# Optimization experiments

Hardware: AMD Instinct MI355X
Metric: run time of the kernel (lower is better)

Reference implementation:

```python
import jax, jax.numpy as jnp
import numpy as np

N = 100000
E = 1600000
IN_DIM = 256
HID = 64


def setup_inputs() -> dict:
    key = jax.random.key(0)
    k1, k2, k3 = jax.random.split(key, 3)
    x = jax.random.normal(k1, (N, IN_DIM), dtype=jnp.float32)
    edge_index = jax.random.randint(k2, (2, E), 0, N, dtype=jnp.int64)
    # glorot-ish init for GCNConv weight, zero bias (PyG default)
    W = jax.random.normal(k3, (IN_DIM, HID), dtype=jnp.float32) * (1.0 / np.sqrt(IN_DIM))
    b = jnp.zeros((HID,), dtype=jnp.float32)
    return {"x": x, "edge_index": edge_index, "W": W, "b": b}


def reference(x, edge_index, W, b):
    # GCNConv: out = D^{-1/2} (A + I) D^{-1/2} (X W) + b
    n = x.shape[0]
    # add self-loops
    loop = jnp.arange(n, dtype=edge_index.dtype)
    src = jnp.concatenate([edge_index[0], loop])  # [E+N]
    dst = jnp.concatenate([edge_index[1], loop])  # [E+N]
    # degree of target nodes (incl. self-loops)
    deg = jax.ops.segment_sum(jnp.ones_like(dst, dtype=x.dtype), dst, num_segments=n)
    dinv = jnp.where(deg > 0, jax.lax.rsqrt(deg), 0.0)  # deg^{-1/2}, inf->0
    norm = dinv[src] * dinv[dst]  # [E+N]
    h = x @ W  # [N, HID] transform before aggregation
    msg = h[src] * norm[:, None]  # gather + scale, [E+N, HID]
    out = jax.ops.segment_sum(msg, dst, num_segments=n)  # scatter-add
    return out + b
```

## Files before the change

kernel.cpp:

```cpp
#include <hip/hip_runtime.h>

typedef float floatx4 __attribute__((ext_vector_type(4)));
typedef short s16x8 __attribute__((ext_vector_type(8)));

#define WG 256
#define NBUCK 512
#define BSH 8
#define EBLK 512
#define CAP 8192

__device__ inline unsigned pack_bf16_rne(float a, float b) {
    unsigned ua = __float_as_uint(a), ub = __float_as_uint(b);
    ua = (ua + 0x7FFFu + ((ua >> 16) & 1u)) >> 16;
    ub = (ub + 0x7FFFu + ((ub >> 16) & 1u)) >> 16;
    return ua | (ub << 16);
}

union FragU {
    unsigned u[4];
    uint4 q;
    s16x8 v;
};

__global__ __launch_bounds__(WG) void k_build(const void* __restrict__ ei, int* __restrict__ cursor,
                                              unsigned* __restrict__ ebuf, int E) {
    __shared__ int h[NBUCK];
    __shared__ int base[NBUCK];
    __shared__ int s32flag;
    const int t = threadIdx.x;
    if (t == 0) s32flag = 0;
    for (int i = t; i < NBUCK; i += WG) h[i] = 0;
    __syncthreads();
    {
        const int* w = (const int*)ei;
        int nz = 0;
        for (int j = t; j < 4096; j += WG) nz |= (w[2 * j + 1] != 0);
        if (nz) atomicOr(&s32flag, 1);
    }
    __syncthreads();
    const bool i32 = (s32flag != 0);
    const int chunk = (E + EBLK - 1) / EBLK;
    const int s = blockIdx.x * chunk;
    const int eend = min(E, s + chunk);
    if (i32) {
        const int* pd = (const int*)ei + E;
        for (int e = s + t; e < eend; e += WG) atomicAdd(&h[pd[e] >> BSH], 1);
    } else {
        const long long* pd = (const long long*)ei + E;
        for (int e = s + t; e < eend; e += WG) atomicAdd(&h[(int)pd[e] >> BSH], 1);
    }
    __syncthreads();
    for (int i = t; i < NBUCK; i += WG) {
        int c = h[i];
        base[i] = c ? atomicAdd(&cursor[i], c) : 0;
        h[i] = 0;
    }
    __syncthreads();
    for (int e = s + t; e < eend; e += WG) {
        int sN, dN;
        if (i32) {
            const int* p = (const int*)ei;
            sN = p[e];
            dN = p[E + e];
        } else {
            const long long* p = (const long long*)ei;
            sN = (int)p[e];
            dN = (int)p[(long long)E + e];
        }
        int bkt = dN >> BSH;
        int pos = base[bkt] + atomicAdd(&h[bkt], 1);
        if (pos < CAP) ebuf[(size_t)bkt * CAP + pos] = (unsigned)sN | ((unsigned)(dN & 255) << 24);
    }
}

__global__ __launch_bounds__(WG) void k_mid(const unsigned* __restrict__ ebuf, const int* __restrict__ cursor,
                                            int* __restrict__ off, int* __restrict__ srcs,
                                            float* __restrict__ dinv,
                                            const float* __restrict__ x, const float* __restrict__ W,
                                            unsigned short* __restrict__ g, int N, int nbuse) {
    __shared__ unsigned smem[2048 * 4];
    const int t = threadIdx.x;

    if ((int)blockIdx.x < nbuse) {
        int* red = (int*)smem;
        int* h = red + 256;
        int* sc = h + 256;
        int* cur = sc + 256;
        const int b = blockIdx.x;
        const int node0 = b << BSH;
        const int rows = min(256, N - node0);
        int part = 0;
        for (int i = t; i < b; i += WG) part += min(cursor[i], CAP);
        red[t] = part;
        h[t] = 0;
        __syncthreads();
        for (int d = WG / 2; d > 0; d >>= 1) {
            if (t < d) red[t] += red[t + d];
            __syncthreads();
        }
        const int ebase = red[0];
        const int cnt = min(cursor[b], CAP);
        const unsigned* eb = ebuf + (size_t)b * CAP;
        for (int j = t; j < cnt; j += WG) atomicAdd(&h[eb[j] >> 24], 1);
        __syncthreads();
        const int deg = (t < rows) ? h[t] + 1 : 0;
        sc[t] = deg;
        __syncthreads();
        for (int d = 1; d < 256; d <<= 1) {
            int a = (t >= d) ? sc[t - d] : 0;
            __syncthreads();
            sc[t] += a;
            __syncthreads();
        }
        const int basef = ebase + node0;
        const int local = sc[t] - deg;
        if (t < rows) {
            off[node0 + t] = basef + local;
            srcs[basef + local] = node0 + t;
            cur[t] = local + 1;
            dinv[node0 + t] = rsqrtf((float)deg);
        }
        if (b == nbuse - 1 && t == 0) off[N] = ebase + cnt + N;
        __syncthreads();
        for (int j = t; j < cnt; j += WG) {
            unsigned w = eb[j];
            int dl = (int)(w >> 24);
            int pos = basef + atomicAdd(&cur[dl], 1);
            srcs[pos] = (int)(w & 0xFFFFFFu);
        }
    } else {
        const int bb = blockIdx.x - nbuse;
        for (int q = t; q < 2048; q += WG) {
            const int kb = q >> 8, nt = (q >> 6) & 3, ln = q & 63;
            const int quad = ln >> 4, l15 = ln & 15;
            const int col = nt * 16 + l15;
            const int krow = kb * 32 + quad * 8;
            unsigned up[4];
#pragma unroll
            for (int p = 0; p < 4; p++) {
                float a = W[(krow + 2 * p) * 64 + col];
                float b2 = W[(krow + 2 * p + 1) * 64 + col];
                up[p] = pack_bf16_rne(a, b2);
            }
            uint4 pk = {up[0], up[1], up[2], up[3]};
            *(uint4*)(&smem[q * 4]) = pk;
        }
        __syncthreads();

        const int wv = t >> 6;
        const int lane = t & 63;
        const int quad = lane >> 4, l15 = lane & 15;

        long long arow = (long long)bb * 64 + wv * 16 + l15;
        if (arow >= N) arow = N - 1;
        const float* xr = x + arow * 256 + quad * 8;

        floatx4 xv[8][2];
#pragma unroll
        for (int kb = 0; kb < 8; kb++) {
            xv[kb][0] = *(const floatx4*)(xr + kb * 32);
            xv[kb][1] = *(const floatx4*)(xr + kb * 32 + 4);
        }

        floatx4 acc[4];
#pragma unroll
        for (int nt = 0; nt < 4; nt++) acc[nt] = 0.f;

#pragma unroll
        for (int kb = 0; kb < 8; kb++) {
            FragU a;
            a.u[0] = pack_bf16_rne(xv[kb][0][0], xv[kb][0][1]);
            a.u[1] = pack_bf16_rne(xv[kb][0][2], xv[kb][0][3]);
            a.u[2] = pack_bf16_rne(xv[kb][1][0], xv[kb][1][1]);
            a.u[3] = pack_bf16_rne(xv[kb][1][2], xv[kb][1][3]);
#pragma unroll
            for (int nt = 0; nt < 4; nt++) {
                FragU b2;
                b2.q = *(const uint4*)(&smem[((kb * 4 + nt) * 64 + lane) * 4]);
                acc[nt] = __builtin_amdgcn_mfma_f32_16x16x32_bf16(a.v, b2.v, acc[nt], 0, 0, 0);
            }
        }

        const long long orow0 = (long long)bb * 64 + wv * 16 + quad * 4;
#pragma unroll
        for (int r = 0; r < 4; r++) {
            const long long orow = orow0 + r;
            if (orow < N) {
#pragma unroll
                for (int nt = 0; nt < 4; nt++) {
                    float v = acc[nt][r];
                    unsigned uv = __float_as_uint(v);
                    uv = (uv + 0x7FFFu + ((uv >> 16) & 1u)) >> 16;
                    g[orow * 64 + nt * 16 + l15] = (unsigned short)uv;
                }
            }
        }
    }
}

__global__ __launch_bounds__(WG) void k_gather(const unsigned short* __restrict__ g,
                                               const int* __restrict__ off, const int* __restrict__ srcs,
                                               const float* __restrict__ dinv, const float* __restrict__ bias,
                                               float* __restrict__ out, int N) {
    int wid = (blockIdx.x * WG + threadIdx.x) >> 6;
    int lane = threadIdx.x & 63;
    if (wid >= N) return;
    int grp = lane >> 3;
    int c8 = (lane & 7) * 8;
    int e0 = off[wid], e1 = off[wid + 1];
    float a0 = 0.f, a1 = 0.f, a2 = 0.f, a3 = 0.f, a4 = 0.f, a5 = 0.f, a6 = 0.f, a7 = 0.f;
    int e = e0 + grp;
    int s = (e < e1) ? srcs[e] : 0;
    while (e < e1) {
        int en = e + 8;
        int sn = (en < e1) ? srcs[en] : 0;
        float ds = dinv[s];
        uint4 v = *(const uint4*)(g + (long long)s * 64 + c8);
        a0 += ds * __uint_as_float(v.x << 16);
        a1 += ds * __uint_as_float(v.x & 0xFFFF0000u);
        a2 += ds * __uint_as_float(v.y << 16);
        a3 += ds * __uint_as_float(v.y & 0xFFFF0000u);
        a4 += ds * __uint_as_float(v.z << 16);
        a5 += ds * __uint_as_float(v.z & 0xFFFF0000u);
        a6 += ds * __uint_as_float(v.w << 16);
        a7 += ds * __uint_as_float(v.w & 0xFFFF0000u);
        s = sn;
        e = en;
    }
#pragma unroll
    for (int m = 8; m <= 32; m <<= 1) {
        a0 += __shfl_xor(a0, m, 64);
        a1 += __shfl_xor(a1, m, 64);
        a2 += __shfl_xor(a2, m, 64);
        a3 += __shfl_xor(a3, m, 64);
        a4 += __shfl_xor(a4, m, 64);
        a5 += __shfl_xor(a5, m, 64);
        a6 += __shfl_xor(a6, m, 64);
        a7 += __shfl_xor(a7, m, 64);
    }
    if (grp == 0) {
        float d = dinv[wid];
        const floatx4 b0 = *(const floatx4*)(bias + c8);
        const floatx4 b1 = *(const floatx4*)(bias + c8 + 4);
        floatx4 o0, o1;
        o0[0] = d * a0 + b0[0];
        o0[1] = d * a1 + b0[1];
        o0[2] = d * a2 + b0[2];
        o0[3] = d * a3 + b0[3];
        o1[0] = d * a4 + b1[0];
        o1[1] = d * a5 + b1[1];
        o1[2] = d * a6 + b1[2];
        o1[3] = d * a7 + b1[3];
        *(floatx4*)(out + (long long)wid * 64 + c8) = o0;
        *(floatx4*)(out + (long long)wid * 64 + c8 + 4) = o1;
    }
}

extern "C" void kernel_launch(void* const* d_in, const int* in_sizes, int n_in,
                              void* d_out, int out_size, void* d_ws, size_t ws_size,
                              hipStream_t stream) {
    const float* x = (const float*)d_in[0];
    const void* ei = d_in[1];
    const float* W = (const float*)d_in[2];
    const float* b = (const float*)d_in[3];
    float* out = (float*)d_out;

    const int N = in_sizes[0] / 256;
    const int E = in_sizes[1] / 2;
    const int NBUSE = (N + 255) >> BSH;
    const int GEMMB = (N + 63) / 64;

    char* ws = (char*)d_ws;
    size_t o = 0;
    auto alloc = [&](size_t bytes) -> void* {
        void* p = ws + o;
        o += (bytes + 255) & ~(size_t)255;
        return p;
    };
    float* dinv = (float*)alloc((size_t)N * 4);
    unsigned short* g = (unsigned short*)alloc((size_t)N * 64 * 2);
    unsigned* ebuf = (unsigned*)alloc((size_t)NBUSE * CAP * 4);
    int* cursor = (int*)alloc((size_t)NBUCK * 4);
    int* off = (int*)alloc((size_t)(N + 1) * 4);
    int* srcs = (int*)alloc((size_t)(E + N) * 4);
    if (o > ws_size) return;

    hipMemsetAsync(cursor, 0, (size_t)NBUCK * 4, stream);
    k_build<<<EBLK, WG, 0, stream>>>(ei, cursor, ebuf, E);
    k_mid<<<NBUSE + GEMMB, WG, 0, stream>>>(ebuf, cursor, off, srcs, dinv, x, W, g, N, NBUSE);
    k_gather<<<(N * 64 + WG - 1) / WG, WG, 0, stream>>>(g, off, srcs, dinv, b, out, N);
}
```

Before: 270.1 us.

## Overlap edge bucketing with GEMM and prepack W in a separate kernel

Reorganizes the launch schedule so the edge bucketing pass runs in the same kernel as the X·W MFMA GEMM blocks, and the CSR construction moves into its own kernel afterward. W is converted to a bf16 MFMA fragment layout once by a small prepack kernel, which also zeroes the cursor array in place of the memset. GEMM blocks then copy the packed W into LDS after issuing their x loads. The aim is to overlap the atomic-heavy bucketing with the bandwidth-heavy GEMM and to stop every GEMM block from repacking W. The cost is one extra kernel launch, and the two kinds of blocks now share one grid.

```diff
diff --git a/kernel.cpp b/kernel.cpp
--- a/kernel.cpp
+++ b/kernel.cpp
@@ -22,131 +22,82 @@
     s16x8 v;
 };
 
-__global__ __launch_bounds__(WG) void k_build(const void* __restrict__ ei, int* __restrict__ cursor,
-                                              unsigned* __restrict__ ebuf, int E) {
-    __shared__ int h[NBUCK];
-    __shared__ int base[NBUCK];
-    __shared__ int s32flag;
-    const int t = threadIdx.x;
-    if (t == 0) s32flag = 0;
-    for (int i = t; i < NBUCK; i += WG) h[i] = 0;
-    __syncthreads();
-    {
-        const int* w = (const int*)ei;
-        int nz = 0;
-        for (int j = t; j < 4096; j += WG) nz |= (w[2 * j + 1] != 0);
-        if (nz) atomicOr(&s32flag, 1);
-    }
-    __syncthreads();
-    const bool i32 = (s32flag != 0);
-    const int chunk = (E + EBLK - 1) / EBLK;
-    const int s = blockIdx.x * chunk;
-    const int eend = min(E, s + chunk);
-    if (i32) {
-        const int* pd = (const int*)ei + E;
-        for (int e = s + t; e < eend; e += WG) atomicAdd(&h[pd[e] >> BSH], 1);
-    } else {
-        const long long* pd = (const long long*)ei + E;
-        for (int e = s + t; e < eend; e += WG) atomicAdd(&h[(int)pd[e] >> BSH], 1);
-    }
-    __syncthreads();
-    for (int i = t; i < NBUCK; i += WG) {
-        int c = h[i];
-        base[i] = c ? atomicAdd(&cursor[i], c) : 0;
-        h[i] = 0;
-    }
-    __syncthreads();
-    for (int e = s + t; e < eend; e += WG) {
-        int sN, dN;
-        if (i32) {
-            const int* p = (const int*)ei;
-            sN = p[e];
-            dN = p[E + e];
-        } else {
-            const long long* p = (const long long*)ei;
-            sN = (int)p[e];
-            dN = (int)p[(long long)E + e];
-        }
-        int bkt = dN >> BSH;
-        int pos = base[bkt] + atomicAdd(&h[bkt], 1);
-        if (pos < CAP) ebuf[(size_t)bkt * CAP + pos] = (unsigned)sN | ((unsigned)(dN & 255) << 24);
-    }
-}
-
-__global__ __launch_bounds__(WG) void k_mid(const unsigned* __restrict__ ebuf, const int* __restrict__ cursor,
-                                            int* __restrict__ off, int* __restrict__ srcs,
-                                            float* __restrict__ dinv,
-                                            const float* __restrict__ x, const float* __restrict__ W,
-                                            unsigned short* __restrict__ g, int N, int nbuse) {
+__global__ __launch_bounds__(WG) void k_packw(const float* __restrict__ W,
+                                              uint4* __restrict__ wpack,
+                                              int* __restrict__ cursor) {
+    const int q = blockIdx.x * WG + threadIdx.x;
+    if (q < NBUCK) cursor[q] = 0;
+    const int kb = q >> 8, nt = (q >> 6) & 3, ln = q & 63;
+    const int quad = ln >> 4, l15 = ln & 15;
+    const int col = nt * 16 + l15;
+    const int krow = kb * 32 + quad * 8;
+    unsigned up[4];
+#pragma unroll
+    for (int p = 0; p < 4; p++) {
+        float a = W[(krow + 2 * p) * 64 + col];
+        float b2 = W[(krow + 2 * p + 1) * 64 + col];
+        up[p] = pack_bf16_rne(a, b2);
+    }
+    uint4 pk = {up[0], up[1], up[2], up[3]};
+    wpack[q] = pk;
+}
+
+__global__ __launch_bounds__(WG) void k_main(const void* __restrict__ ei, int* __restrict__ cursor,
+                                             unsigned* __restrict__ ebuf, int E,
+                                             const float* __restrict__ x, const uint4* __restrict__ wpack,
+                                             unsigned short* __restrict__ g, int N) {
     __shared__ unsigned smem[2048 * 4];
     const int t = threadIdx.x;
 
-    if ((int)blockIdx.x < nbuse) {
-        int* red = (int*)smem;
-        int* h = red + 256;
-        int* sc = h + 256;
-        int* cur = sc + 256;
-        const int b = blockIdx.x;
-        const int node0 = b << BSH;
-        const int rows = min(256, N - node0);
-        int part = 0;
-        for (int i = t; i < b; i += WG) part += min(cursor[i], CAP);
-        red[t] = part;
-        h[t] = 0;
-        __syncthreads();
-        for (int d = WG / 2; d > 0; d >>= 1) {
-            if (t < d) red[t] += red[t + d];
-            __syncthreads();
-        }
-        const int ebase = red[0];
-        const int cnt = min(cursor[b], CAP);
-        const unsigned* eb = ebuf + (size_t)b * CAP;
-        for (int j = t; j < cnt; j += WG) atomicAdd(&h[eb[j] >> 24], 1);
-        __syncthreads();
-        const int deg = (t < rows) ? h[t] + 1 : 0;
-        sc[t] = deg;
-        __syncthreads();
-        for (int d = 1; d < 256; d <<= 1) {
-            int a = (t >= d) ? sc[t - d] : 0;
-            __syncthreads();
-            sc[t] += a;
-            __syncthreads();
-        }
-        const int basef = ebase + node0;
-        const int local = sc[t] - deg;
-        if (t < rows) {
-            off[node0 + t] = basef + local;
-            srcs[basef + local] = node0 + t;
-            cur[t] = local + 1;
-            dinv[node0 + t] = rsqrtf((float)deg);
-        }
-        if (b == nbuse - 1 && t == 0) off[N] = ebase + cnt + N;
-        __syncthreads();
-        for (int j = t; j < cnt; j += WG) {
-            unsigned w = eb[j];
-            int dl = (int)(w >> 24);
-            int pos = basef + atomicAdd(&cur[dl], 1);
-            srcs[pos] = (int)(w & 0xFFFFFFu);
+    if ((int)blockIdx.x < EBLK) {
+        int* h = (int*)smem;
+        int* base = h + NBUCK;
+        int* s32flag = base + NBUCK;
+        if (t == 0) *s32flag = 0;
+        for (int i = t; i < NBUCK; i += WG) h[i] = 0;
+        __syncthreads();
+        {
+            const int* w = (const int*)ei;
+            int nz = 0;
+            for (int j = t; j < 4096; j += WG) nz |= (w[2 * j + 1] != 0);
+            if (nz) atomicOr(s32flag, 1);
+        }
+        __syncthreads();
+        const bool i32 = (*s32flag != 0);
+        const int chunk = (E + EBLK - 1) / EBLK;
+        const int s = blockIdx.x * chunk;
+        const int eend = min(E, s + chunk);
+        if (i32) {
+            const int* pd = (const int*)ei + E;
+            for (int e = s + t; e < eend; e += WG) atomicAdd(&h[pd[e] >> BSH], 1);
+        } else {
+            const long long* pd = (const long long*)ei + E;
+            for (int e = s + t; e < eend; e += WG) atomicAdd(&h[(int)pd[e] >> BSH], 1);
+        }
+        __syncthreads();
+        for (int i = t; i < NBUCK; i += WG) {
+            int c = h[i];
+            base[i] = c ? atomicAdd(&cursor[i], c) : 0;
+            h[i] = 0;
+        }
+        __syncthreads();
+        for (int e = s + t; e < eend; e += WG) {
+            int sN, dN;
+            if (i32) {
+                const int* p = (const int*)ei;
+                sN = p[e];
+                dN = p[E + e];
+            } else {
+                const long long* p = (const long long*)ei;
+                sN = (int)p[e];
+                dN = (int)p[(long long)E + e];
+            }
+            int bkt = dN >> BSH;
+            int pos = base[bkt] + atomicAdd(&h[bkt], 1);
+            if (pos < CAP) ebuf[(size_t)bkt * CAP + pos] = (unsigned)sN | ((unsigned)(dN & 255) << 24);
         }
     } else {
-        const int bb = blockIdx.x - nbuse;
-        for (int q = t; q < 2048; q += WG) {
-            const int kb = q >> 8, nt = (q >> 6) & 3, ln = q & 63;
-            const int quad = ln >> 4, l15 = ln & 15;
-            const int col = nt * 16 + l15;
-            const int krow = kb * 32 + quad * 8;
-            unsigned up[4];
-#pragma unroll
-            for (int p = 0; p < 4; p++) {
-                float a = W[(krow + 2 * p) * 64 + col];
-                float b2 = W[(krow + 2 * p + 1) * 64 + col];
-                up[p] = pack_bf16_rne(a, b2);
-            }
-            uint4 pk = {up[0], up[1], up[2], up[3]};
-            *(uint4*)(&smem[q * 4]) = pk;
-        }
-        __syncthreads();
-
+        const int bb = blockIdx.x - EBLK;
         const int wv = t >> 6;
         const int lane = t & 63;
         const int quad = lane >> 4, l15 = lane & 15;
@@ -161,6 +112,14 @@
             xv[kb][0] = *(const floatx4*)(xr + kb * 32);
             xv[kb][1] = *(const floatx4*)(xr + kb * 32 + 4);
         }
+        __builtin_amdgcn_sched_barrier(0);
+
+#pragma unroll
+        for (int i = 0; i < 8; i++) {
+            const int q = i * WG + t;
+            ((uint4*)smem)[q] = wpack[q];
+        }
+        __syncthreads();
 
         floatx4 acc[4];
 #pragma unroll
@@ -195,6 +154,58 @@
                 }
             }
         }
+    }
+}
+
+__global__ __launch_bounds__(WG) void k_csr(const unsigned* __restrict__ ebuf, const int* __restrict__ cursor,
+                                            int* __restrict__ off, int* __restrict__ srcs,
+                                            float* __restrict__ dinv, int N, int nbuse) {
+    __shared__ int red[256];
+    __shared__ int h[256];
+    __shared__ int sc[256];
+    __shared__ int cur[256];
+    const int t = threadIdx.x;
+    const int b = blockIdx.x;
+    const int node0 = b << BSH;
+    const int rows = min(256, N - node0);
+    int part = 0;
+    for (int i = t; i < b; i += WG) part += min(cursor[i], CAP);
+    red[t] = part;
+    h[t] = 0;
+    __syncthreads();
+    for (int d = WG / 2; d > 0; d >>= 1) {
+        if (t < d) red[t] += red[t + d];
+        __syncthreads();
+    }
+    const int ebase = red[0];
+    const int cnt = min(cursor[b], CAP);
+    const unsigned* eb = ebuf + (size_t)b * CAP;
+    for (int j = t; j < cnt; j += WG) atomicAdd(&h[eb[j] >> 24], 1);
+    __syncthreads();
+    const int deg = (t < rows) ? h[t] + 1 : 0;
+    sc[t] = deg;
+    __syncthreads();
+    for (int d = 1; d < 256; d <<= 1) {
+        int a = (t >= d) ? sc[t - d] : 0;
+        __syncthreads();
+        sc[t] += a;
+        __syncthreads();
+    }
+    const int basef = ebase + node0;
+    const int local = sc[t] - deg;
+    if (t < rows) {
+        off[node0 + t] = basef + local;
+        srcs[basef + local] = node0 + t;
+        cur[t] = local + 1;
+        dinv[node0 + t] = rsqrtf((float)deg);
+    }
+    if (b == nbuse - 1 && t == 0) off[N] = ebase + cnt + N;
+    __syncthreads();
+    for (int j = t; j < cnt; j += WG) {
+        unsigned w = eb[j];
+        int dl = (int)(w >> 24);
+        int pos = basef + atomicAdd(&cur[dl], 1);
+        srcs[pos] = (int)(w & 0xFFFFFFu);
     }
 }
 
@@ -283,10 +294,11 @@
     int* cursor = (int*)alloc((size_t)NBUCK * 4);
     int* off = (int*)alloc((size_t)(N + 1) * 4);
     int* srcs = (int*)alloc((size_t)(E + N) * 4);
+    uint4* wpack = (uint4*)alloc((size_t)2048 * 16);
     if (o > ws_size) return;
 
-    hipMemsetAsync(cursor, 0, (size_t)NBUCK * 4, stream);
-    k_build<<<EBLK, WG, 0, stream>>>(ei, cursor, ebuf, E);
-    k_mid<<<NBUSE + GEMMB, WG, 0, stream>>>(ebuf, cursor, off, srcs, dinv, x, W, g, N, NBUSE);
+    k_packw<<<8, WG, 0, stream>>>(W, wpack, cursor);
+    k_main<<<EBLK + GEMMB, WG, 0, stream>>>(ei, cursor, ebuf, E, x, wpack, g, N);
+    k_csr<<<NBUSE, WG, 0, stream>>>(ebuf, cursor, off, srcs, dinv, N, NBUSE);
     k_gather<<<(N * 64 + WG - 1) / WG, WG, 0, stream>>>(g, off, srcs, dinv, b, out, N);
 }
```

Result: faster. 258.4 us (-4.4%).
